# Performance work log

Measured on AMD Instinct MI355X. Metric: run time of the kernel, lower is better.

Reference implementation:

```python
import jax, jax.numpy as jnp
import numpy as np

B, DIN, HID, COMP = 16384, 1024, 512, 64

def setup_inputs() -> dict:
    key = jax.random.key(0)
    ks = jax.random.split(key, 16)
    s = lambda fan_in: 1.0 / np.sqrt(fan_in)
    return {
        "x1": jax.random.normal(ks[0], (B, DIN), jnp.float32),
        "x2": jax.random.normal(ks[1], (B, DIN), jnp.float32),
        "Wb1": jax.random.normal(ks[2], (DIN, HID), jnp.float32) * s(DIN),
        "bb1": jnp.zeros((HID,), jnp.float32),
        "Wb2": jax.random.normal(ks[3], (DIN, HID), jnp.float32) * s(DIN),
        "bb2": jnp.zeros((HID,), jnp.float32),
        "Wc1": jax.random.normal(ks[4], (HID, COMP), jnp.float32) * s(HID),
        "bc1": jnp.zeros((COMP,), jnp.float32),
        "Wc2": jax.random.normal(ks[5], (HID, COMP), jnp.float32) * s(HID),
        "bc2": jnp.zeros((COMP,), jnp.float32),
        "Wf1": jax.random.normal(ks[6], (COMP * COMP, 64), jnp.float32) * s(COMP * COMP),
        "bf1": jnp.zeros((64,), jnp.float32),
        "Wf2": jax.random.normal(ks[7], (64, 2), jnp.float32) * s(64),
        "bf2": jnp.zeros((2,), jnp.float32),
    }

def reference(x1, x2, Wb1, bb1, Wb2, bb2, Wc1, bc1, Wc2, bc2, Wf1, bf1, Wf2, bf2):
    # branch + compress: [B, DIN] -> [B, HID] -> [B, COMP]
    f1 = (jax.nn.relu(x1 @ Wb1 + bb1)) @ Wc1 + bc1  # [B, 64]
    f2 = (jax.nn.relu(x2 @ Wb2 + bb2)) @ Wc2 + bc2  # [B, 64]
    # kronecker_product(f1, f2): per-sample (f2 col) * (f1 row) -> [64,64], row-major flatten
    # element at flat index p*64 + q is f2[p] * f1[q]
    kron = jnp.einsum('bp,bq->bpq', f2, f1).reshape(f1.shape[0], -1)  # [B, 4096]
    h = kron @ Wf1 + bf1   # [B, 64]
    out = h @ Wf2 + bf2    # [B, 2]
    return out
```

## Files before the change

kernel.cpp:

```cpp
#include <hip/hip_runtime.h>

#define B_SZ 16384
#define DIN  1024
#define HID  512
#define COMP 64

typedef __bf16 bf16_t;
typedef __bf16 bf16x4 __attribute__((ext_vector_type(4)));
typedef __bf16 bf16x8 __attribute__((ext_vector_type(8)));
typedef float  f32x4  __attribute__((ext_vector_type(4)));

#define MFMA16 __builtin_amdgcn_mfma_f32_16x16x32_bf16

__device__ __forceinline__ void gl2lds16(const void* g, void* l) {
    __builtin_amdgcn_global_load_lds(
        (const __attribute__((address_space(1))) void*)g,
        (__attribute__((address_space(3))) void*)l, 16, 0, 0);
}

__global__ __launch_bounds__(256) void k_prep(
    const float* __restrict__ Wb1, const float* __restrict__ Wb2,
    bf16_t* __restrict__ wbt1, bf16_t* __restrict__ wbt2,
    const float* __restrict__ Wc1, const float* __restrict__ Wc2,
    bf16_t* __restrict__ wct1, bf16_t* __restrict__ wct2,
    const float* __restrict__ Wf1, const float* __restrict__ bf1v,
    const float* __restrict__ Wf2, const float* __restrict__ bf2v,
    const float* __restrict__ bc1, const float* __restrict__ bc2,
    float* __restrict__ f1, float* __restrict__ f2,
    const float* __restrict__ x1, const float* __restrict__ x2,
    bf16_t* __restrict__ xb1, bf16_t* __restrict__ xb2,
    float* __restrict__ G, float* __restrict__ c)
{
    const int bid = blockIdx.x, tid = threadIdx.x;

    if (bid >= 3152) {
        const int i0 = (bid - 3152) * 256 + tid;
        #pragma unroll
        for (int k = 0; k < 8; k++) {
            const float* x  = (k < 4) ? x1  : x2;
            bf16_t*      xb = (k < 4) ? xb2 : xb2;
            xb = (k < 4) ? xb1 : xb2;
            const size_t ch = (size_t)i0 + (size_t)(k & 3) * 524288;
            const size_t base = ch * 8;
            float4 v0 = *reinterpret_cast<const float4*>(x + base);
            float4 v1 = *reinterpret_cast<const float4*>(x + base + 4);
            bf16x8 o;
            o[0] = (bf16_t)v0.x; o[1] = (bf16_t)v0.y;
            o[2] = (bf16_t)v0.z; o[3] = (bf16_t)v0.w;
            o[4] = (bf16_t)v1.x; o[5] = (bf16_t)v1.y;
            o[6] = (bf16_t)v1.z; o[7] = (bf16_t)v1.w;
            *reinterpret_cast<bf16x8*>(xb + base) = o;
        }
        return;
    }

    __shared__ float tile[32][33];
    const int tx = tid & 31, ty = tid >> 5;

    if (bid < 1024) {
        const int z = bid >> 9, t = bid & 511;
        const float* in  = z ? Wb2  : Wb1;
        bf16_t*      out = z ? wbt2 : wbt1;
        const int n0 = (t & 15) * 32, k0 = (t >> 4) * 32;
        #pragma unroll
        for (int i = 0; i < 4; i++)
            tile[ty + i * 8][tx] = in[(size_t)(k0 + ty + i * 8) * HID + n0 + tx];
        __syncthreads();
        #pragma unroll
        for (int i = 0; i < 4; i++)
            out[(size_t)(n0 + ty + i * 8) * DIN + k0 + tx] = (bf16_t)tile[tx][ty + i * 8];
    } else if (bid < 1088) {
        const int l = bid - 1024;
        const int z = l >> 5, t = l & 31;
        const float* in  = z ? Wc2  : Wc1;
        bf16_t*      out = z ? wct2 : wct1;
        const int n0 = (t & 1) * 32, k0 = (t >> 1) * 32;
        #pragma unroll
        for (int i = 0; i < 4; i++)
            tile[ty + i * 8][tx] = in[(size_t)(k0 + ty + i * 8) * COMP + n0 + tx];
        __syncthreads();
        #pragma unroll
        for (int i = 0; i < 4; i++)
            out[(size_t)(n0 + ty + i * 8) * HID + k0 + tx] = (bf16_t)tile[tx][ty + i * 8];
    } else if (bid < 1104) {
        const int i = (bid - 1088) * 256 + tid;
        float a0 = 0.f, a1 = 0.f;
        #pragma unroll 8
        for (int o = 0; o < 64; o++) {
            float w = Wf1[(size_t)i * 64 + o];
            a0 = fmaf(w, Wf2[o * 2 + 0], a0);
            a1 = fmaf(w, Wf2[o * 2 + 1], a1);
        }
        G[i]        = a0;
        G[4096 + i] = a1;
        if (i < 2) {
            float s = bf2v[i];
            for (int o = 0; o < 64; o++) s = fmaf(bf1v[o], Wf2[o * 2 + i], s);
            c[i] = s;
        }
    } else {
        const int l = bid - 1104;
        const int z = l >> 10;
        const float* bc = z ? bc2 : bc1;
        float*       f  = z ? f2  : f1;
        const int i = (l & 1023) * 256 + tid;
        const int c4 = (i & 15) * 4;
        float4 v = make_float4(bc[c4], bc[c4 + 1], bc[c4 + 2], bc[c4 + 3]);
        reinterpret_cast<float4*>(f)[i] = v;
    }
}

__global__ __launch_bounds__(512, 2) void k_gemm1f(
    const bf16_t* __restrict__ XB1, const bf16_t* __restrict__ XB2,
    const bf16_t* __restrict__ WT1, const bf16_t* __restrict__ WT2,
    const float* __restrict__ bias1, const float* __restrict__ bias2,
    const bf16_t* __restrict__ WC1, const bf16_t* __restrict__ WC2,
    float* __restrict__ F1, float* __restrict__ F2)
{
    const int bid = blockIdx.x;
    const int nid = (bid & 7) * 32 + (bid >> 3);
    const int z   = nid >> 7;
    const int nb  = (nid >> 6) & 1;
    const int mb  = nid & 63;

    const bf16_t* XB   = z ? XB2   : XB1;
    const bf16_t* WT   = z ? WT2   : WT1;
    const float*  bias = z ? bias2 : bias1;
    const bf16_t* WC   = z ? WC2   : WC1;
    float*        F    = z ? F2    : F1;

    const int m0 = mb * 256;
    const int n0 = nb * 256;

    __shared__ __align__(128) char smem[135168];

    const int tid  = threadIdx.x;
    const int lane = tid & 63;
    const int wave = tid >> 6;
    const int wm   = wave >> 2;
    const int wn   = wave & 3;
    const int l15  = lane & 15;
    const int g4   = lane >> 4;

    const int srow = tid >> 3;
    const int sch  = (tid & 7) ^ (srow & 7);
    const bf16_t* gA = XB + (size_t)(m0 + srow) * DIN + sch * 8;
    const bf16_t* gB = WT + (size_t)(n0 + srow) * DIN + sch * 8;
    const int ldst = tid * 16;

    const int l7   = l15 & 7;
    const int lch0 = (g4 ^ l7) * 16;
    const int lch1 = ((4 + g4) ^ l7) * 16;
    const int abase = (wm * 64 + l15) * 128;
    const int bbase = (wn * 64 + l15) * 128;

    f32x4 acc[2][4][4] = {};

    gl2lds16(gA,                        smem + ldst);
    gl2lds16(gA + (size_t)64 * DIN,     smem + 8192 + ldst);
    gl2lds16(gA + (size_t)128 * DIN,    smem + 16384 + ldst);
    gl2lds16(gA + (size_t)192 * DIN,    smem + 24576 + ldst);
    gl2lds16(gB,                        smem + 65536 + ldst);
    gl2lds16(gB + (size_t)64 * DIN,     smem + 65536 + 8192 + ldst);
    gl2lds16(gB + (size_t)128 * DIN,    smem + 65536 + 16384 + ldst);
    gl2lds16(gB + (size_t)192 * DIN,    smem + 65536 + 24576 + ldst);
    gl2lds16(gA + 64,                   smem + 32768 + ldst);
    gl2lds16(gA + 64 + (size_t)64 * DIN, smem + 32768 + 8192 + ldst);
    __builtin_amdgcn_sched_barrier(0);

    #pragma unroll 1
    for (int kt = 0; kt < 16; ++kt) {
        const int d = kt & 1;
        const char* Ac = smem + d * 32768;
        const char* Bc = smem + 65536 + d * 32768;
        char* An = (char*)smem + (d ^ 1) * 32768;
        char* Bn = (char*)smem + 65536 + (d ^ 1) * 32768;
        char* An2 = (char*)smem + d * 32768;
        const bf16_t* gA1 = gA + (kt + 1) * 64;
        const bf16_t* gA2 = gA + (kt + 2) * 64;
        const bf16_t* gB1 = gB + (kt + 1) * 64;

        gl2lds16(gA1 + (size_t)128 * DIN, An + 16384 + ldst);
        gl2lds16(gA1 + (size_t)192 * DIN, An + 24576 + ldst);
        gl2lds16(gB1,                     Bn + ldst);
        gl2lds16(gB1 + (size_t)64 * DIN,  Bn + 8192 + ldst);
        gl2lds16(gB1 + (size_t)128 * DIN, Bn + 16384 + ldst);
        gl2lds16(gB1 + (size_t)192 * DIN, Bn + 24576 + ldst);
        __builtin_amdgcn_sched_barrier(0);
        asm volatile("s_waitcnt vmcnt(8)" ::: "memory");
        __builtin_amdgcn_s_barrier();
        __builtin_amdgcn_sched_barrier(0);

        bf16x8 a[4][2], b[4][2];
        #pragma unroll
        for (int mi = 0; mi < 4; mi++) {
            a[mi][0] = *(const bf16x8*)(Ac + abase + mi * 2048 + lch0);
            a[mi][1] = *(const bf16x8*)(Ac + abase + mi * 2048 + lch1);
        }
        #pragma unroll
        for (int ni = 0; ni < 4; ni++) {
            b[ni][0] = *(const bf16x8*)(Bc + bbase + ni * 2048 + lch0);
            b[ni][1] = *(const bf16x8*)(Bc + bbase + ni * 2048 + lch1);
        }
        __builtin_amdgcn_s_setprio(1);
        #pragma unroll
        for (int mi = 0; mi < 4; mi++)
            #pragma unroll
            for (int ni = 0; ni < 4; ni++) {
                acc[0][mi][ni] = MFMA16(a[mi][0], b[ni][0], acc[0][mi][ni], 0, 0, 0);
                acc[0][mi][ni] = MFMA16(a[mi][1], b[ni][1], acc[0][mi][ni], 0, 0, 0);
            }
        __builtin_amdgcn_s_setprio(0);
        __builtin_amdgcn_sched_barrier(0);
        __builtin_amdgcn_s_barrier();
        __builtin_amdgcn_sched_barrier(0);

        gl2lds16(gA2,                     An2 + ldst);
        gl2lds16(gA2 + (size_t)64 * DIN,  An2 + 8192 + ldst);
        __builtin_amdgcn_sched_barrier(0);

        bf16x8 a2[4][2];
        #pragma unroll
        for (int mi = 0; mi < 4; mi++) {
            a2[mi][0] = *(const bf16x8*)(Ac + 16384 + abase + mi * 2048 + lch0);
            a2[mi][1] = *(const bf16x8*)(Ac + 16384 + abase + mi * 2048 + lch1);
        }
        __builtin_amdgcn_s_setprio(1);
        #pragma unroll
        for (int mi = 0; mi < 4; mi++)
            #pragma unroll
            for (int ni = 0; ni < 4; ni++) {
                acc[1][mi][ni] = MFMA16(a2[mi][0], b[ni][0], acc[1][mi][ni], 0, 0, 0);
                acc[1][mi][ni] = MFMA16(a2[mi][1], b[ni][1], acc[1][mi][ni], 0, 0, 0);
            }
        __builtin_amdgcn_s_setprio(0);
        __builtin_amdgcn_sched_barrier(0);
        __builtin_amdgcn_s_barrier();
        __builtin_amdgcn_sched_barrier(0);
    }

    asm volatile("s_waitcnt vmcnt(0)" ::: "memory");
    __builtin_amdgcn_s_barrier();

    bf16_t* Hs = (bf16_t*)smem;
    float bv[4];
    #pragma unroll
    for (int ni = 0; ni < 4; ni++)
        bv[ni] = bias[n0 + wn * 64 + ni * 16 + l15];
    #pragma unroll
    for (int ph = 0; ph < 2; ph++) {
        #pragma unroll
        for (int mi = 0; mi < 4; mi++) {
            const int lr = ph * 128 + wm * 64 + mi * 16 + g4 * 4;
            #pragma unroll
            for (int ni = 0; ni < 4; ni++) {
                const int colL = wn * 64 + ni * 16 + l15;
                #pragma unroll
                for (int r = 0; r < 4; r++) {
                    float v = fmaxf(acc[ph][mi][ni][r] + bv[ni], 0.0f);
                    Hs[(lr + r) * 264 + colL] = (bf16_t)v;
                }
            }
        }
    }
    __syncthreads();

    f32x4 acc2[2][4] = {};
    #pragma unroll
    for (int kk = 0; kk < 256; kk += 32) {
        bf16x8 af2[2];
        #pragma unroll
        for (int m2 = 0; m2 < 2; m2++)
            af2[m2] = *(const bf16x8*)(Hs + (wave * 32 + m2 * 16 + l15) * 264 + kk + g4 * 8);
        #pragma unroll
        for (int ni = 0; ni < 4; ni++) {
            bf16x8 bw = *(const bf16x8*)(&WC[(size_t)(ni * 16 + l15) * HID + n0 + kk + g4 * 8]);
            #pragma unroll
            for (int m2 = 0; m2 < 2; m2++)
                acc2[m2][ni] = MFMA16(af2[m2], bw, acc2[m2][ni], 0, 0, 0);
        }
    }
    #pragma unroll
    for (int m2 = 0; m2 < 2; m2++) {
        const int rbase = m0 + wave * 32 + m2 * 16 + g4 * 4;
        #pragma unroll
        for (int ni = 0; ni < 4; ni++) {
            const int col = ni * 16 + l15;
            #pragma unroll
            for (int r = 0; r < 4; r++)
                unsafeAtomicAdd(&F[(size_t)(rbase + r) * COMP + col], acc2[m2][ni][r]);
        }
    }
}

__global__ __launch_bounds__(256) void k_bilinear(
    const float* __restrict__ f1, const float* __restrict__ f2,
    const float* __restrict__ G, const float* __restrict__ c,
    float* __restrict__ out)
{
    __shared__ float Gs[2][4096];
    __shared__ float f1t[64][66];
    __shared__ float f2t[64][66];
    __shared__ float part[4][64];

    const int tid = threadIdx.x;
    const int s0  = blockIdx.x * 64;

    for (int i = tid; i < 2048; i += 256)
        reinterpret_cast<float4*>(&Gs[0][0])[i] =
            reinterpret_cast<const float4*>(G)[i];

    #pragma unroll
    for (int rr = 0; rr < 4; rr++) {
        const int row = (tid >> 4) + rr * 16;
        const int c4  = (tid & 15) * 4;
        float4 v1 = *reinterpret_cast<const float4*>(&f1[(size_t)(s0 + row) * 64 + c4]);
        float4 v2 = *reinterpret_cast<const float4*>(&f2[(size_t)(s0 + row) * 64 + c4]);
        f1t[c4 + 0][row] = v1.x; f1t[c4 + 1][row] = v1.y;
        f1t[c4 + 2][row] = v1.z; f1t[c4 + 3][row] = v1.w;
        f2t[c4 + 0][row] = v2.x; f2t[c4 + 1][row] = v2.y;
        f2t[c4 + 2][row] = v2.z; f2t[c4 + 3][row] = v2.w;
    }
    __syncthreads();

    const int lane = tid & 63;
    const int wv   = tid >> 6;
    const int j    = wv & 1;
    const int qh   = (wv >> 1) * 32;

    float tq[32];
    #pragma unroll
    for (int q = 0; q < 32; q++) tq[q] = 0.f;

    #pragma unroll 4
    for (int p = 0; p < 64; p++) {
        const float f2p = f2t[p][lane];
        const float* Gp = &Gs[j][p * 64 + qh];
        #pragma unroll
        for (int q4 = 0; q4 < 8; q4++) {
            float4 g = *reinterpret_cast<const float4*>(Gp + q4 * 4);
            tq[q4 * 4 + 0] = fmaf(f2p, g.x, tq[q4 * 4 + 0]);
            tq[q4 * 4 + 1] = fmaf(f2p, g.y, tq[q4 * 4 + 1]);
            tq[q4 * 4 + 2] = fmaf(f2p, g.z, tq[q4 * 4 + 2]);
            tq[q4 * 4 + 3] = fmaf(f2p, g.w, tq[q4 * 4 + 3]);
        }
    }

    float o = 0.f;
    #pragma unroll
    for (int q = 0; q < 32; q++)
        o = fmaf(f1t[qh + q][lane], tq[q], o);

    part[wv][lane] = o;
    __syncthreads();

    if (wv < 2) {
        float r = part[wv][lane] + part[wv + 2][lane] + c[wv];
        out[(size_t)(s0 + lane) * 2 + wv] = r;
    }
}

extern "C" void kernel_launch(void* const* d_in, const int* in_sizes, int n_in,
                              void* d_out, int out_size, void* d_ws, size_t ws_size,
                              hipStream_t stream)
{
    const float* x1  = (const float*)d_in[0];
    const float* x2  = (const float*)d_in[1];
    const float* Wb1 = (const float*)d_in[2];
    const float* bb1 = (const float*)d_in[3];
    const float* Wb2 = (const float*)d_in[4];
    const float* bb2 = (const float*)d_in[5];
    const float* Wc1 = (const float*)d_in[6];
    const float* bc1 = (const float*)d_in[7];
    const float* Wc2 = (const float*)d_in[8];
    const float* bc2 = (const float*)d_in[9];
    const float* Wf1 = (const float*)d_in[10];
    const float* bf1v = (const float*)d_in[11];
    const float* Wf2 = (const float*)d_in[12];
    const float* bf2v = (const float*)d_in[13];
    float* out = (float*)d_out;

    char* ws = (char*)d_ws;
    bf16_t* wbt1 = (bf16_t*)ws; ws += (size_t)HID * DIN * 2;
    bf16_t* wbt2 = (bf16_t*)ws; ws += (size_t)HID * DIN * 2;
    bf16_t* wct1 = (bf16_t*)ws; ws += (size_t)COMP * HID * 2;
    bf16_t* wct2 = (bf16_t*)ws; ws += (size_t)COMP * HID * 2;
    bf16_t* xb1  = (bf16_t*)ws; ws += (size_t)B_SZ * DIN * 2;
    bf16_t* xb2  = (bf16_t*)ws; ws += (size_t)B_SZ * DIN * 2;
    float*  f1   = (float*)ws;  ws += (size_t)B_SZ * COMP * 4;
    float*  f2   = (float*)ws;  ws += (size_t)B_SZ * COMP * 4;
    float*  G    = (float*)ws;  ws += (size_t)2 * 4096 * 4;
    float*  c    = (float*)ws;  ws += 256;

    k_prep<<<5200, 256, 0, stream>>>(Wb1, Wb2, wbt1, wbt2,
                                     Wc1, Wc2, wct1, wct2,
                                     Wf1, bf1v, Wf2, bf2v,
                                     bc1, bc2, f1, f2,
                                     x1, x2, xb1, xb2, G, c);
    k_gemm1f<<<256, 512, 0, stream>>>(xb1, xb2, wbt1, wbt2, bb1, bb2,
                                      wct1, wct2, f1, f2);
    k_bilinear<<<256, 256, 0, stream>>>(f1, f2, G, c, out);
}
```

Baseline: 243.7 us.

## Fuse fp32-to-bf16 input conversion into GEMM A-tile loading via register staging

Removes the separate pass in the prep kernel that converted x1/x2 to bf16 in a workspace. The first GEMM now reads fp32 inputs directly into registers, converts them to bf16 and writes them to LDS, while B tiles keep using direct global-to-LDS loads. The K-loop is reorganised so these register-staged loads are interleaved with the MFMA phases, with adjusted waitcnt and barrier points. This removes the bf16 workspace write and its later re-read. In exchange, each fp32 row is read by both N-blocks (twice the bytes per A load), the A path loses its async direct-to-LDS load, and register pressure rises.

```diff
diff --git a/kernel.cpp b/kernel.cpp
--- a/kernel.cpp
+++ b/kernel.cpp
@@ -16,6 +16,15 @@
     __builtin_amdgcn_global_load_lds(
         (const __attribute__((address_space(1))) void*)g,
         (__attribute__((address_space(3))) void*)l, 16, 0, 0);
+}
+
+__device__ __forceinline__ bf16x8 cvt8(float4 a, float4 b) {
+    bf16x8 o;
+    o[0] = (bf16_t)a.x; o[1] = (bf16_t)a.y;
+    o[2] = (bf16_t)a.z; o[3] = (bf16_t)a.w;
+    o[4] = (bf16_t)b.x; o[5] = (bf16_t)b.y;
+    o[6] = (bf16_t)b.z; o[7] = (bf16_t)b.w;
+    return o;
 }
 
 __global__ __launch_bounds__(256) void k_prep(
@@ -27,32 +36,9 @@
     const float* __restrict__ Wf2, const float* __restrict__ bf2v,
     const float* __restrict__ bc1, const float* __restrict__ bc2,
     float* __restrict__ f1, float* __restrict__ f2,
-    const float* __restrict__ x1, const float* __restrict__ x2,
-    bf16_t* __restrict__ xb1, bf16_t* __restrict__ xb2,
     float* __restrict__ G, float* __restrict__ c)
 {
     const int bid = blockIdx.x, tid = threadIdx.x;
-
-    if (bid >= 3152) {
-        const int i0 = (bid - 3152) * 256 + tid;
-        #pragma unroll
-        for (int k = 0; k < 8; k++) {
-            const float* x  = (k < 4) ? x1  : x2;
-            bf16_t*      xb = (k < 4) ? xb2 : xb2;
-            xb = (k < 4) ? xb1 : xb2;
-            const size_t ch = (size_t)i0 + (size_t)(k & 3) * 524288;
-            const size_t base = ch * 8;
-            float4 v0 = *reinterpret_cast<const float4*>(x + base);
-            float4 v1 = *reinterpret_cast<const float4*>(x + base + 4);
-            bf16x8 o;
-            o[0] = (bf16_t)v0.x; o[1] = (bf16_t)v0.y;
-            o[2] = (bf16_t)v0.z; o[3] = (bf16_t)v0.w;
-            o[4] = (bf16_t)v1.x; o[5] = (bf16_t)v1.y;
-            o[6] = (bf16_t)v1.z; o[7] = (bf16_t)v1.w;
-            *reinterpret_cast<bf16x8*>(xb + base) = o;
-        }
-        return;
-    }
 
     __shared__ float tile[32][33];
     const int tx = tid & 31, ty = tid >> 5;
@@ -111,7 +97,7 @@
 }
 
 __global__ __launch_bounds__(512, 2) void k_gemm1f(
-    const bf16_t* __restrict__ XB1, const bf16_t* __restrict__ XB2,
+    const float* __restrict__ X1, const float* __restrict__ X2,
     const bf16_t* __restrict__ WT1, const bf16_t* __restrict__ WT2,
     const float* __restrict__ bias1, const float* __restrict__ bias2,
     const bf16_t* __restrict__ WC1, const bf16_t* __restrict__ WC2,
@@ -123,7 +109,7 @@
     const int nb  = (nid >> 6) & 1;
     const int mb  = nid & 63;
 
-    const bf16_t* XB   = z ? XB2   : XB1;
+    const float*  X    = z ? X2    : X1;
     const bf16_t* WT   = z ? WT2   : WT1;
     const float*  bias = z ? bias2 : bias1;
     const bf16_t* WC   = z ? WC2   : WC1;
@@ -144,7 +130,7 @@
 
     const int srow = tid >> 3;
     const int sch  = (tid & 7) ^ (srow & 7);
-    const bf16_t* gA = XB + (size_t)(m0 + srow) * DIN + sch * 8;
+    const float*  gX = X  + (size_t)(m0 + srow) * DIN + sch * 8;
     const bf16_t* gB = WT + (size_t)(n0 + srow) * DIN + sch * 8;
     const int ldst = tid * 16;
 
@@ -155,17 +141,29 @@
     const int bbase = (wn * 64 + l15) * 128;
 
     f32x4 acc[2][4][4] = {};
-
-    gl2lds16(gA,                        smem + ldst);
-    gl2lds16(gA + (size_t)64 * DIN,     smem + 8192 + ldst);
-    gl2lds16(gA + (size_t)128 * DIN,    smem + 16384 + ldst);
-    gl2lds16(gA + (size_t)192 * DIN,    smem + 24576 + ldst);
-    gl2lds16(gB,                        smem + 65536 + ldst);
-    gl2lds16(gB + (size_t)64 * DIN,     smem + 65536 + 8192 + ldst);
-    gl2lds16(gB + (size_t)128 * DIN,    smem + 65536 + 16384 + ldst);
-    gl2lds16(gB + (size_t)192 * DIN,    smem + 65536 + 24576 + ldst);
-    gl2lds16(gA + 64,                   smem + 32768 + ldst);
-    gl2lds16(gA + 64 + (size_t)64 * DIN, smem + 32768 + 8192 + ldst);
+    float4 r0, r1, r2, r3;
+
+    #pragma unroll
+    for (int u = 0; u < 4; u++)
+        gl2lds16(gB + (size_t)u * 64 * DIN, smem + 65536 + u * 8192 + ldst);
+    r0 = *(const float4*)(gX);
+    r1 = *(const float4*)(gX + 4);
+    r2 = *(const float4*)(gX + (size_t)64 * DIN);
+    r3 = *(const float4*)(gX + (size_t)64 * DIN + 4);
+    *(bf16x8*)(smem + ldst)        = cvt8(r0, r1);
+    *(bf16x8*)(smem + 8192 + ldst) = cvt8(r2, r3);
+    r0 = *(const float4*)(gX + (size_t)128 * DIN);
+    r1 = *(const float4*)(gX + (size_t)128 * DIN + 4);
+    r2 = *(const float4*)(gX + (size_t)192 * DIN);
+    r3 = *(const float4*)(gX + (size_t)192 * DIN + 4);
+    *(bf16x8*)(smem + 16384 + ldst)        = cvt8(r0, r1);
+    *(bf16x8*)(smem + 16384 + 8192 + ldst) = cvt8(r2, r3);
+    r0 = *(const float4*)(gX + 64);
+    r1 = *(const float4*)(gX + 64 + 4);
+    r2 = *(const float4*)(gX + (size_t)64 * DIN + 64);
+    r3 = *(const float4*)(gX + (size_t)64 * DIN + 64 + 4);
+    asm volatile("s_waitcnt lgkmcnt(0)" ::: "memory");
+    __builtin_amdgcn_s_barrier();
     __builtin_amdgcn_sched_barrier(0);
 
     #pragma unroll 1
@@ -175,20 +173,20 @@
         const char* Bc = smem + 65536 + d * 32768;
         char* An = (char*)smem + (d ^ 1) * 32768;
         char* Bn = (char*)smem + 65536 + (d ^ 1) * 32768;
-        char* An2 = (char*)smem + d * 32768;
-        const bf16_t* gA1 = gA + (kt + 1) * 64;
-        const bf16_t* gA2 = gA + (kt + 2) * 64;
-        const bf16_t* gB1 = gB + (kt + 1) * 64;
-
-        gl2lds16(gA1 + (size_t)128 * DIN, An + 16384 + ldst);
-        gl2lds16(gA1 + (size_t)192 * DIN, An + 24576 + ldst);
-        gl2lds16(gB1,                     Bn + ldst);
-        gl2lds16(gB1 + (size_t)64 * DIN,  Bn + 8192 + ldst);
-        gl2lds16(gB1 + (size_t)128 * DIN, Bn + 16384 + ldst);
-        gl2lds16(gB1 + (size_t)192 * DIN, Bn + 24576 + ldst);
-        __builtin_amdgcn_sched_barrier(0);
-        asm volatile("s_waitcnt vmcnt(8)" ::: "memory");
-        __builtin_amdgcn_s_barrier();
+        const int kb  = (kt < 15 ? kt + 1 : 15) * 64;
+        const int kc1 = kb;
+        const int kc2 = (kt < 14 ? kt + 2 : 15) * 64;
+
+        gl2lds16(gB + (size_t)0 * 64 * DIN + kb, Bn + 0 * 8192 + ldst);
+        gl2lds16(gB + (size_t)1 * 64 * DIN + kb, Bn + 1 * 8192 + ldst);
+        __builtin_amdgcn_sched_barrier(0);
+        *(bf16x8*)(An + ldst)        = cvt8(r0, r1);
+        *(bf16x8*)(An + 8192 + ldst) = cvt8(r2, r3);
+        __builtin_amdgcn_sched_barrier(0);
+        r0 = *(const float4*)(gX + (size_t)128 * DIN + kc1);
+        r1 = *(const float4*)(gX + (size_t)128 * DIN + kc1 + 4);
+        r2 = *(const float4*)(gX + (size_t)192 * DIN + kc1);
+        r3 = *(const float4*)(gX + (size_t)192 * DIN + kc1 + 4);
         __builtin_amdgcn_sched_barrier(0);
 
         bf16x8 a[4][2], b[4][2];
@@ -212,11 +210,20 @@
             }
         __builtin_amdgcn_s_setprio(0);
         __builtin_amdgcn_sched_barrier(0);
+        asm volatile("s_waitcnt lgkmcnt(0)" ::: "memory");
         __builtin_amdgcn_s_barrier();
         __builtin_amdgcn_sched_barrier(0);
 
-        gl2lds16(gA2,                     An2 + ldst);
-        gl2lds16(gA2 + (size_t)64 * DIN,  An2 + 8192 + ldst);
+        gl2lds16(gB + (size_t)2 * 64 * DIN + kb, Bn + 2 * 8192 + ldst);
+        gl2lds16(gB + (size_t)3 * 64 * DIN + kb, Bn + 3 * 8192 + ldst);
+        __builtin_amdgcn_sched_barrier(0);
+        *(bf16x8*)(An + 16384 + ldst)        = cvt8(r0, r1);
+        *(bf16x8*)(An + 16384 + 8192 + ldst) = cvt8(r2, r3);
+        __builtin_amdgcn_sched_barrier(0);
+        r0 = *(const float4*)(gX + kc2);
+        r1 = *(const float4*)(gX + kc2 + 4);
+        r2 = *(const float4*)(gX + (size_t)64 * DIN + kc2);
+        r3 = *(const float4*)(gX + (size_t)64 * DIN + kc2 + 4);
         __builtin_amdgcn_sched_barrier(0);
 
         bf16x8 a2[4][2];
@@ -235,11 +242,12 @@
             }
         __builtin_amdgcn_s_setprio(0);
         __builtin_amdgcn_sched_barrier(0);
+        asm volatile("s_waitcnt vmcnt(4) lgkmcnt(0)" ::: "memory");
         __builtin_amdgcn_s_barrier();
         __builtin_amdgcn_sched_barrier(0);
     }
 
-    asm volatile("s_waitcnt vmcnt(0)" ::: "memory");
+    asm volatile("s_waitcnt vmcnt(0) lgkmcnt(0)" ::: "memory");
     __builtin_amdgcn_s_barrier();
 
     bf16_t* Hs = (bf16_t*)smem;
@@ -385,19 +393,16 @@
     bf16_t* wbt2 = (bf16_t*)ws; ws += (size_t)HID * DIN * 2;
     bf16_t* wct1 = (bf16_t*)ws; ws += (size_t)COMP * HID * 2;
     bf16_t* wct2 = (bf16_t*)ws; ws += (size_t)COMP * HID * 2;
-    bf16_t* xb1  = (bf16_t*)ws; ws += (size_t)B_SZ * DIN * 2;
-    bf16_t* xb2  = (bf16_t*)ws; ws += (size_t)B_SZ * DIN * 2;
     float*  f1   = (float*)ws;  ws += (size_t)B_SZ * COMP * 4;
     float*  f2   = (float*)ws;  ws += (size_t)B_SZ * COMP * 4;
     float*  G    = (float*)ws;  ws += (size_t)2 * 4096 * 4;
     float*  c    = (float*)ws;  ws += 256;
 
-    k_prep<<<5200, 256, 0, stream>>>(Wb1, Wb2, wbt1, wbt2,
+    k_prep<<<3152, 256, 0, stream>>>(Wb1, Wb2, wbt1, wbt2,
                                      Wc1, Wc2, wct1, wct2,
                                      Wf1, bf1v, Wf2, bf2v,
-                                     bc1, bc2, f1, f2,
-                                     x1, x2, xb1, xb2, G, c);
-    k_gemm1f<<<256, 512, 0, stream>>>(xb1, xb2, wbt1, wbt2, bb1, bb2,
+                                     bc1, bc2, f1, f2, G, c);
+    k_gemm1f<<<256, 512, 0, stream>>>(x1, x2, wbt1, wbt2, bb1, bb2,
                                       wct1, wct2, f1, f2);
     k_bilinear<<<256, 256, 0, stream>>>(f1, f2, G, c, out);
 }
```

After: 224.2 us. -8.0%, faster.
